# Kernel tuning notes

Hardware: AMD Instinct MI355X
Metric: run time of the kernel (lower is better)

## Reference

```python
import jax, jax.numpy as jnp
import numpy as np

N = 65536
R = 9          # num_relations + 1
D_IN = 256
D_HID = 512
D_OUT = 256
N_HIDDEN = 2


def _xavier(key, shape):
    fan_out, fan_in = shape[-2], shape[-1]
    limit = np.sqrt(6.0 / (fan_in + fan_out))
    return jax.random.uniform(key, shape, jnp.float32, -limit, limit)


def setup_inputs() -> dict:
    key = jax.random.key(0)
    ks = jax.random.split(key, 12)
    inp = {
        "x": jax.random.normal(ks[0], (N, D_IN), jnp.float32),
        "edge_attr": jax.random.uniform(ks[1], (N, R), jnp.float32),
    }
    dims = [(D_HID, D_IN)] + [(D_HID, D_HID)] * N_HIDDEN + [(D_OUT, D_HID)]
    for i, (o, ii) in enumerate(dims):
        inp[f"W{i}"] = _xavier(ks[2 + 2 * i], (R, o, ii))
        inp[f"b{i}"] = _xavier(ks[3 + 2 * i], (R, o))
    return inp


def _linear_kg(x, edge_attr, W, b):
    # roi,ni,nr->no : relation-mixed linear per node
    y = jnp.einsum("roi,ni,nr->no", W, x, edge_attr)
    return y + edge_attr @ b


def reference(x, edge_attr, W0, b0, W1, b1, W2, b2, W3, b3):
    y = jax.nn.relu(_linear_kg(x, edge_attr, W0, b0))
    y = jax.nn.relu(_linear_kg(y, edge_attr, W1, b1))
    y = jax.nn.relu(_linear_kg(y, edge_attr, W2, b2))
    y = _linear_kg(y, edge_attr, W3, b3)
    return y
```

## Files before the change

kernel.cpp:

```cpp
#include <hip/hip_runtime.h>
#include <stdint.h>

using f32x4  = __attribute__((ext_vector_type(4))) float;
using bf16x8 = __attribute__((ext_vector_type(8))) __bf16;

#define GLOAD_LDS16(src, dst) __builtin_amdgcn_global_load_lds(                 \
    (const __attribute__((address_space(1))) void*)(src),                      \
    (__attribute__((address_space(3))) void*)(dst), 16, 0, 0)


__global__ void cvt_x_kernel(const float* __restrict__ x, __bf16* __restrict__ out) {
    const int u    = blockIdx.x * 256 + threadIdx.x;
    const int lane = u & 63;
    const int f    = (u >> 6) & 31;
    const int c    = (u >> 11) & 1;
    const int rb   = u >> 12;
    const int row  = rb * 128 + ((f >> 2) << 4) + (lane & 15);
    const int i    = c * 128 + ((f & 3) << 5) + ((lane >> 4) << 3);
    const float4 a = *(const float4*)(x + (size_t)row * 256 + i);
    const float4 b = *(const float4*)(x + (size_t)row * 256 + i + 4);
    bf16x8 pv;
    pv[0] = (__bf16)a.x; pv[1] = (__bf16)a.y; pv[2] = (__bf16)a.z; pv[3] = (__bf16)a.w;
    pv[4] = (__bf16)b.x; pv[5] = (__bf16)b.y; pv[6] = (__bf16)b.z; pv[7] = (__bf16)b.w;
    *(bf16x8*)(out + (size_t)u * 8) = pv;
}

template<int I, int O>
__global__ void prep_w_kernel(const float* __restrict__ W, __bf16* __restrict__ Bt) {
    constexpr int NCH = I >> 7;
    const int u    = blockIdx.x * 256 + threadIdx.x;
    const int r    = blockIdx.y;
    const int nb   = blockIdx.z;
    const int lane = u & 63;
    const int g    = (u >> 6) & 15;
    const int h    = (u >> 10) & 1;
    const int c    = u >> 11;
    const int mi   = g >> 1;
    const int ks   = (h << 1) + (g & 1);
    const int row  = nb * 128 + mi * 16 + (lane & 15);
    const int i    = c * 128 + ks * 32 + ((lane >> 4) << 3);
    const float* src = W + ((size_t)r * O + row) * I + i;
    const float4 a = *(const float4*)src;
    const float4 b = *(const float4*)(src + 4);
    bf16x8 pv;
    pv[0] = (__bf16)a.x; pv[1] = (__bf16)a.y; pv[2] = (__bf16)a.z; pv[3] = (__bf16)a.w;
    pv[4] = (__bf16)b.x; pv[5] = (__bf16)b.y; pv[6] = (__bf16)b.z; pv[7] = (__bf16)b.w;
    *(bf16x8*)(Bt + ((((size_t)nb * 9 + r) * NCH + c) * 2048 + (u & 2047)) * 8) = pv;
}

template<int O>
__global__ void prep_bias_kernel(const float* __restrict__ b, __bf16* __restrict__ BtB) {
    const int u    = blockIdx.x * 256 + threadIdx.x;
    const int nb   = u >> 10;
    const int q    = u & 1023;
    const int lane = q & 63;
    const int f    = q >> 6;
    const int row  = nb * 128 + ((f >> 1) << 4) + (lane & 15);
    const int kb   = ((f & 1) << 5) + ((lane >> 4) << 3);
    bf16x8 pv;
#pragma unroll
    for (int e = 0; e < 8; ++e) {
        const int k = kb + e;
        pv[e] = (k < 9) ? (__bf16)b[(size_t)k * O + row] : (__bf16)0.f;
    }
    *(bf16x8*)(BtB + (size_t)u * 8) = pv;
}

template<int I, int O, bool RELU, bool OUTF32>
__global__ __launch_bounds__(256, 2)
void kg_gemm(const __bf16* __restrict__ A, const float* __restrict__ E,
             const __bf16* __restrict__ Bt, const __bf16* __restrict__ BtB,
             void* __restrict__ Outv) {
    constexpr int NCH = I >> 7;
    constexpr int NBN = O >> 7;
    static_assert((I & 127) == 0 && (O & 127) == 0, "tile divisibility");

    __shared__ __align__(16) char lds[32768 + 2 * 16384 + 4608];
    char*  const ldsA  = lds;
    char*  const ldsB0 = lds + 32768;
    char*  const ldsB1 = lds + 49152;
    float* const ldsE  = (float*)(lds + 65536);

    const int tid  = threadIdx.x;
    const int nwg  = gridDim.x;
    const int braw = blockIdx.x;
    const int bid  = (braw & 7) * (nwg >> 3) + (braw >> 3);
    const int rb   = bid / NBN;
    const int nb   = bid % NBN;
    const int bm0  = rb << 7;
    const int bn0  = nb << 7;
    const int lane = tid & 63;
    const int wid  = tid >> 6;
    const int wr   = (wid >> 1) << 6;
    const int wc   = (wid & 1) << 6;
    const int l15  = lane & 15;
    const int lq   = lane >> 4;

    if (tid < 128) {
        const float* e = E + (size_t)(bm0 + tid) * 9;
#pragma unroll
        for (int q = 0; q < 9; ++q) ldsE[q * 128 + tid] = e[q];
    }

    f32x4 acc[4][4];
#pragma unroll
    for (int m = 0; m < 4; ++m)
#pragma unroll
        for (int n = 0; n < 4; ++n)
            acc[m][n] = f32x4{0.f, 0.f, 0.f, 0.f};
    const f32x4 zero4 = {0.f, 0.f, 0.f, 0.f};

    const size_t Abase = (size_t)rb * NCH * 2048;
    const size_t Bbase = (size_t)nb * 9 * NCH * 2048;
    const int afb = (wr >> 4) << 2;
    const int nfb = (wc >> 4) << 1;

    auto stageA = [&](int c) {
        const __bf16* src = A + (Abase + (size_t)c * 2048) * 8;
#pragma unroll
        for (int rr = 0; rr < 8; ++rr) {
            const int q = rr * 256 + tid;
            GLOAD_LDS16(src + (size_t)q * 8, ldsA + q * 16);
        }
    };
    auto stageBh = [&](int r, int c, char* dst, int h) {
        const __bf16* src = Bt + (Bbase + ((size_t)r * NCH + c) * 2048 + (size_t)(h << 10)) * 8;
#pragma unroll
        for (int it = 0; it < 4; ++it) {
            const int q = it * 256 + tid;
            GLOAD_LDS16(src + (size_t)q * 8, dst + q * 16);
        }
    };

#pragma unroll 1
    for (int c = 0; c < NCH; ++c) {
        asm volatile("s_waitcnt lgkmcnt(0)" ::: "memory");
        __builtin_amdgcn_s_barrier();
        __builtin_amdgcn_sched_barrier(0);
        stageA(c);
        stageBh(0, c, ldsB0, 0);
        stageBh(0, c, ldsB1, 1);
#pragma unroll 1
        for (int r = 0; r < 9; ++r) {
            f32x4 acc2[4][4];
#pragma unroll
            for (int h = 0; h < 2; ++h) {
                char* const buf = h ? ldsB1 : ldsB0;
                if (r == 8 && h == 1) asm volatile("s_waitcnt vmcnt(0)" ::: "memory");
                else                  asm volatile("s_waitcnt vmcnt(4)" ::: "memory");
                __builtin_amdgcn_s_barrier();
                __builtin_amdgcn_sched_barrier(0);
                bf16x8 bv[4][2];
#pragma unroll
                for (int n = 0; n < 4; ++n)
#pragma unroll
                    for (int j = 0; j < 2; ++j)
                        bv[n][j] = *(const bf16x8*)(buf + (((nfb + 2 * n + j) << 6) + lane) * 16);
                asm volatile("s_waitcnt lgkmcnt(0)" ::: "memory");
                __builtin_amdgcn_sched_barrier(0);
                __builtin_amdgcn_s_barrier();
                __builtin_amdgcn_sched_barrier(0);
                if (r < 8) stageBh(r + 1, c, buf, h);
                bf16x8 av[4][2];
#pragma unroll
                for (int m = 0; m < 4; ++m)
#pragma unroll
                    for (int j = 0; j < 2; ++j)
                        av[m][j] = *(const bf16x8*)(ldsA + (((afb + (m << 2) + 2 * h + j) << 6) + lane) * 16);
                __builtin_amdgcn_s_setprio(1);
#pragma unroll
                for (int j = 0; j < 2; ++j)
#pragma unroll
                    for (int m = 0; m < 4; ++m)
#pragma unroll
                        for (int n = 0; n < 4; ++n)
                            acc2[m][n] = __builtin_amdgcn_mfma_f32_16x16x32_bf16(
                                av[m][j], bv[n][j],
                                (h == 0 && j == 0) ? zero4 : acc2[m][n], 0, 0, 0);
                __builtin_amdgcn_s_setprio(0);
            }
#pragma unroll
            for (int m = 0; m < 4; ++m) {
                const f32x4 ev = *(const f32x4*)(ldsE + r * 128 + wr + m * 16 + lq * 4);
#pragma unroll
                for (int n = 0; n < 4; ++n)
#pragma unroll
                    for (int j = 0; j < 4; ++j)
                        acc[m][n][j] += ev[j] * acc2[m][n][j];
            }
        }
    }

    __syncthreads();
    {
#pragma unroll
        for (int rr = 0; rr < 4; ++rr) {
            const int q = rr * 256 + tid;
            GLOAD_LDS16(BtB + ((size_t)nb * 1024 + q) * 8, ldsB0 + q * 16);
        }
#pragma unroll
        for (int rr = 0; rr < 4; ++rr) {
            const int q    = rr * 256 + tid;
            const int ln   = q & 63;
            const int f    = q >> 6;
            const int row  = ((f >> 1) << 4) + (ln & 15);
            const int kb   = ((f & 1) << 5) + ((ln >> 4) << 3);
            bf16x8 pv;
#pragma unroll
            for (int e8 = 0; e8 < 8; ++e8) {
                const int k = kb + e8;
                pv[e8] = (k < 9) ? (__bf16)ldsE[k * 128 + row] : (__bf16)0.f;
            }
            *(bf16x8*)(ldsA + q * 16) = pv;
        }
        __syncthreads();
#pragma unroll
        for (int ks = 0; ks < 2; ++ks) {
            bf16x8 av[4], bv[4];
#pragma unroll
            for (int m = 0; m < 4; ++m)
                av[m] = *(const bf16x8*)(ldsA + (((((wr >> 4) + m) * 2 + ks) << 6) + lane) * 16);
#pragma unroll
            for (int n = 0; n < 4; ++n)
                bv[n] = *(const bf16x8*)(ldsB0 + (((((wc >> 4) + n) * 2 + ks) << 6) + lane) * 16);
#pragma unroll
            for (int m = 0; m < 4; ++m)
#pragma unroll
                for (int n = 0; n < 4; ++n)
                    acc[m][n] = __builtin_amdgcn_mfma_f32_16x16x32_bf16(
                        av[m], bv[n], acc[m][n], 0, 0, 0);
        }
    }

    if (OUTF32) {
        const int orow0 = bm0 + wr + lq * 4;
        const int ocol0 = bn0 + wc + l15;
#pragma unroll
        for (int m = 0; m < 4; ++m)
#pragma unroll
            for (int n = 0; n < 4; ++n)
#pragma unroll
                for (int j = 0; j < 4; ++j) {
                    float v = acc[m][n][j];
                    if (RELU) v = fmaxf(v, 0.f);
                    ((float*)Outv)[(size_t)(orow0 + m * 16 + j) * O + (ocol0 + n * 16)] = v;
                }
    } else {
        constexpr int NCHn = O >> 7;
        __bf16* outp = (__bf16*)Outv;
#pragma unroll
        for (int m = 0; m < 4; ++m) {
#pragma unroll
            for (int n = 0; n < 4; ++n) {
                const int col  = bn0 + wc + n * 16 + l15;
                const int c2   = col >> 7;
                const int f2   = (((wr >> 4) + m) << 2) + ((col >> 5) & 3);
                const int ln2  = ((col >> 3) & 3) * 16 + lq * 4;
                const size_t base =
                    (((size_t)rb * NCHn + c2) * 2048 + f2 * 64 + ln2) * 8 + (col & 7);
#pragma unroll
                for (int j = 0; j < 4; ++j) {
                    float v = acc[m][n][j];
                    if (RELU) v = fmaxf(v, 0.f);
                    outp[base + (size_t)j * 8] = (__bf16)v;
                }
            }
        }
    }
}

extern "C" void kernel_launch(void* const* d_in, const int* in_sizes, int n_in,
                              void* d_out, int out_size, void* d_ws, size_t ws_size,
                              hipStream_t stream) {
    const float* x  = (const float*)d_in[0];
    const float* E  = (const float*)d_in[1];
    const float* W0 = (const float*)d_in[2];
    const float* b0 = (const float*)d_in[3];
    const float* W1 = (const float*)d_in[4];
    const float* b1 = (const float*)d_in[5];
    const float* W2 = (const float*)d_in[6];
    const float* b2 = (const float*)d_in[7];
    const float* W3 = (const float*)d_in[8];
    const float* b3 = (const float*)d_in[9];

    char* ws = (char*)d_ws;
    const size_t actBytes = (size_t)65536 * 512 * 2;
    __bf16* actA = (__bf16*)ws;
    __bf16* actB = (__bf16*)(ws + actBytes);
    char* p = ws + 2 * actBytes;
    __bf16* Bt0 = (__bf16*)p; p += (size_t)4 * 9 * 2 * 2048 * 16;
    __bf16* Bt1 = (__bf16*)p; p += (size_t)4 * 9 * 4 * 2048 * 16;
    __bf16* Bt2 = (__bf16*)p; p += (size_t)4 * 9 * 4 * 2048 * 16;
    __bf16* Bt3 = (__bf16*)p; p += (size_t)2 * 9 * 4 * 2048 * 16;
    __bf16* BtB0 = (__bf16*)p; p += (size_t)4 * 1024 * 16;
    __bf16* BtB1 = (__bf16*)p; p += (size_t)4 * 1024 * 16;
    __bf16* BtB2 = (__bf16*)p; p += (size_t)4 * 1024 * 16;
    __bf16* BtB3 = (__bf16*)p; p += (size_t)2 * 1024 * 16;
    if (ws_size < (size_t)(p - ws)) return;

    cvt_x_kernel<<<dim3(8192), dim3(256), 0, stream>>>(x, actA);
    prep_w_kernel<256, 512><<<dim3(16, 9, 4), dim3(256), 0, stream>>>(W0, Bt0);
    prep_w_kernel<512, 512><<<dim3(32, 9, 4), dim3(256), 0, stream>>>(W1, Bt1);
    prep_w_kernel<512, 512><<<dim3(32, 9, 4), dim3(256), 0, stream>>>(W2, Bt2);
    prep_w_kernel<512, 256><<<dim3(32, 9, 2), dim3(256), 0, stream>>>(W3, Bt3);
    prep_bias_kernel<512><<<dim3(16), dim3(256), 0, stream>>>(b0, BtB0);
    prep_bias_kernel<512><<<dim3(16), dim3(256), 0, stream>>>(b1, BtB1);
    prep_bias_kernel<512><<<dim3(16), dim3(256), 0, stream>>>(b2, BtB2);
    prep_bias_kernel<256><<<dim3(8),  dim3(256), 0, stream>>>(b3, BtB3);

    kg_gemm<256, 512, true,  false><<<dim3(2048), dim3(256), 0, stream>>>(actA, E, Bt0, BtB0, actB);
    kg_gemm<512, 512, true,  false><<<dim3(2048), dim3(256), 0, stream>>>(actB, E, Bt1, BtB1, actA);
    kg_gemm<512, 512, true,  false><<<dim3(2048), dim3(256), 0, stream>>>(actA, E, Bt2, BtB2, actB);
    kg_gemm<512, 256, false, true ><<<dim3(1024), dim3(256), 0, stream>>>(actB, E, Bt3, BtB3, d_out);
}
```

Baseline: 837.9 us.

## Hold A fragments in registers and deepen B-tile ring to four stages

The A chunk for each K slice now goes straight from global memory into per-wave registers (16 bf16x8 fragments) and is no longer staged through LDS and re-read for every relation. The freed LDS becomes a four-slot ring for B half-tiles, so B is prefetched two stages ahead and vmcnt waits are adjusted to match. This is meant to cut LDS read traffic and hide more global latency. The cost is more VGPR pressure under launch_bounds(256,2), which could cause spills or lower occupancy, and the A loads are now plain global loads that the waits must also cover.

Result: no change. 839.8 us (+0.2%).

```diff
diff --git a/kernel.cpp b/kernel.cpp
--- a/kernel.cpp
+++ b/kernel.cpp
@@ -75,11 +75,8 @@
     constexpr int NBN = O >> 7;
     static_assert((I & 127) == 0 && (O & 127) == 0, "tile divisibility");
 
-    __shared__ __align__(16) char lds[32768 + 2 * 16384 + 4608];
-    char*  const ldsA  = lds;
-    char*  const ldsB0 = lds + 32768;
-    char*  const ldsB1 = lds + 49152;
-    float* const ldsE  = (float*)(lds + 65536);
+    __shared__ __align__(16) char lds[4 * 16384 + 4608];
+    float* const ldsE = (float*)(lds + 65536);
 
     const int tid  = threadIdx.x;
     const int nwg  = gridDim.x;
@@ -115,16 +112,10 @@
     const int afb = (wr >> 4) << 2;
     const int nfb = (wc >> 4) << 1;
 
-    auto stageA = [&](int c) {
-        const __bf16* src = A + (Abase + (size_t)c * 2048) * 8;
-#pragma unroll
-        for (int rr = 0; rr < 8; ++rr) {
-            const int q = rr * 256 + tid;
-            GLOAD_LDS16(src + (size_t)q * 8, ldsA + q * 16);
-        }
-    };
-    auto stageBh = [&](int r, int c, char* dst, int h) {
-        const __bf16* src = Bt + (Bbase + ((size_t)r * NCH + c) * 2048 + (size_t)(h << 10)) * 8;
+    auto stageS = [&](int s, int c) {
+        const __bf16* src = Bt + (Bbase + ((size_t)(s >> 1) * NCH + c) * 2048
+                                  + (size_t)((s & 1) << 10)) * 8;
+        char* dst = lds + ((s & 3) << 14);
 #pragma unroll
         for (int it = 0; it < 4; ++it) {
             const int q = it * 256 + tid;
@@ -137,36 +128,44 @@
         asm volatile("s_waitcnt lgkmcnt(0)" ::: "memory");
         __builtin_amdgcn_s_barrier();
         __builtin_amdgcn_sched_barrier(0);
-        stageA(c);
-        stageBh(0, c, ldsB0, 0);
-        stageBh(0, c, ldsB1, 1);
+        bf16x8 af[4][4];
+        {
+            const __bf16* Ab = A + (Abase + (size_t)c * 2048) * 8;
+#pragma unroll
+            for (int m = 0; m < 4; ++m)
+#pragma unroll
+                for (int ks = 0; ks < 4; ++ks)
+                    af[m][ks] = *(const bf16x8*)(Ab + ((size_t)((afb + (m << 2) + ks) << 6) + lane) * 8);
+        }
+        stageS(0, c); stageS(1, c); stageS(2, c); stageS(3, c);
 #pragma unroll 1
         for (int r = 0; r < 9; ++r) {
             f32x4 acc2[4][4];
 #pragma unroll
             for (int h = 0; h < 2; ++h) {
-                char* const buf = h ? ldsB1 : ldsB0;
-                if (r == 8 && h == 1) asm volatile("s_waitcnt vmcnt(0)" ::: "memory");
-                else                  asm volatile("s_waitcnt vmcnt(4)" ::: "memory");
+                const int s = 2 * r + h;
+                if (h == 0) {
+                    if (r < 8) asm volatile("s_waitcnt vmcnt(12)" ::: "memory");
+                    else       asm volatile("s_waitcnt vmcnt(4)"  ::: "memory");
+                } else {
+                    if (r < 7)      asm volatile("s_waitcnt vmcnt(12)" ::: "memory");
+                    else if (r == 7) asm volatile("s_waitcnt vmcnt(8)" ::: "memory");
+                    else            asm volatile("s_waitcnt vmcnt(0)"  ::: "memory");
+                }
                 __builtin_amdgcn_s_barrier();
                 __builtin_amdgcn_sched_barrier(0);
+                const char* bp = lds + ((s & 3) << 14);
                 bf16x8 bv[4][2];
 #pragma unroll
                 for (int n = 0; n < 4; ++n)
 #pragma unroll
                     for (int j = 0; j < 2; ++j)
-                        bv[n][j] = *(const bf16x8*)(buf + (((nfb + 2 * n + j) << 6) + lane) * 16);
+                        bv[n][j] = *(const bf16x8*)(bp + (((nfb + 2 * n + j) << 6) + lane) * 16);
                 asm volatile("s_waitcnt lgkmcnt(0)" ::: "memory");
                 __builtin_amdgcn_sched_barrier(0);
                 __builtin_amdgcn_s_barrier();
                 __builtin_amdgcn_sched_barrier(0);
-                if (r < 8) stageBh(r + 1, c, buf, h);
-                bf16x8 av[4][2];
-#pragma unroll
-                for (int m = 0; m < 4; ++m)
-#pragma unroll
-                    for (int j = 0; j < 2; ++j)
-                        av[m][j] = *(const bf16x8*)(ldsA + (((afb + (m << 2) + 2 * h + j) << 6) + lane) * 16);
+                if (r < 7) stageS(s + 4, c);
                 __builtin_amdgcn_s_setprio(1);
 #pragma unroll
                 for (int j = 0; j < 2; ++j)
@@ -175,7 +174,7 @@
 #pragma unroll
                         for (int n = 0; n < 4; ++n)
                             acc2[m][n] = __builtin_amdgcn_mfma_f32_16x16x32_bf16(
-                                av[m][j], bv[n][j],
+                                af[m][2 * h + j], bv[n][j],
                                 (h == 0 && j == 0) ? zero4 : acc2[m][n], 0, 0, 0);
                 __builtin_amdgcn_s_setprio(0);
             }
@@ -193,10 +192,12 @@
 
     __syncthreads();
     {
+        char* const bufB = lds;
+        char* const bufA = lds + 16384;
 #pragma unroll
         for (int rr = 0; rr < 4; ++rr) {
             const int q = rr * 256 + tid;
-            GLOAD_LDS16(BtB + ((size_t)nb * 1024 + q) * 8, ldsB0 + q * 16);
+            GLOAD_LDS16(BtB + ((size_t)nb * 1024 + q) * 8, bufB + q * 16);
         }
 #pragma unroll
         for (int rr = 0; rr < 4; ++rr) {
@@ -211,7 +212,7 @@
                 const int k = kb + e8;
                 pv[e8] = (k < 9) ? (__bf16)ldsE[k * 128 + row] : (__bf16)0.f;
             }
-            *(bf16x8*)(ldsA + q * 16) = pv;
+            *(bf16x8*)(bufA + q * 16) = pv;
         }
         __syncthreads();
 #pragma unroll
@@ -219,10 +220,10 @@
             bf16x8 av[4], bv[4];
 #pragma unroll
             for (int m = 0; m < 4; ++m)
-                av[m] = *(const bf16x8*)(ldsA + (((((wr >> 4) + m) * 2 + ks) << 6) + lane) * 16);
+                av[m] = *(const bf16x8*)(bufA + (((((wr >> 4) + m) * 2 + ks) << 6) + lane) * 16);
 #pragma unroll
             for (int n = 0; n < 4; ++n)
-                bv[n] = *(const bf16x8*)(ldsB0 + (((((wc >> 4) + n) * 2 + ks) << 6) + lane) * 16);
+                bv[n] = *(const bf16x8*)(bufB + (((((wc >> 4) + n) * 2 + ks) << 6) + lane) * 16);
 #pragma unroll
             for (int m = 0; m < 4; ++m)
 #pragma unroll
```
